# Kernel tuning notes

Hardware: AMD Instinct MI355X
Metric: run time of the kernel (lower is better)

Reference implementation:

```python
import jax, jax.numpy as jnp
import numpy as np
from jax import lax

NL, H, E, N, R, K, C, V, P = 8, 768, 1536, 16, 4, 4, 3, 256, 2048
EPS = 1e-5

def layernorm(x, w, b):
    m = jnp.mean(x, -1, keepdims=True)
    v = jnp.var(x, -1, keepdims=True)
    return (x - m) * lax.rsqrt(v + EPS) * w + b

def causal_dwconv(x, w, b):
    # x: [B,L,E], w: [E,K], b: [E]; causal depthwise conv (pad K-1 left, truncate)
    Bn, L, _ = x.shape
    xp = jnp.pad(x, ((0, 0), (K - 1, 0), (0, 0)))
    y = b
    acc = jnp.zeros_like(x)
    for j in range(K):
        acc = acc + xp[:, j:j + L, :] * w[:, j]
    return acc + b

def selective_scan(u, dt, Bm, Cm, A, Dv):
    # u,dt: [B,L,E]; Bm,Cm: [B,L,N]; A: [E,N]; Dv: [E]
    Bn = u.shape[0]
    def step(h, inp):
        u_t, dt_t, b_t, c_t = inp  # [B,E],[B,E],[B,N],[B,N]
        dA = jnp.exp(dt_t[:, :, None] * A)                      # [B,E,N]
        h = h * dA + (dt_t * u_t)[:, :, None] * b_t[:, None, :]
        y = jnp.einsum('ben,bn->be', h, c_t)
        return h, y
    h0 = jnp.zeros((Bn, E, N), dtype=u.dtype)
    xs = (u.transpose(1, 0, 2), dt.transpose(1, 0, 2),
          Bm.transpose(1, 0, 2), Cm.transpose(1, 0, 2))
    _, ys = lax.scan(step, h0, xs)
    return ys.transpose(1, 0, 2) + u * Dv

def mamba_block(hs, p):
    res = hs
    x = layernorm(hs, p['ln_w'], p['ln_b'])
    proj = x @ p['in_w'] + p['in_b']                            # [B,L,2E]
    xm, gate = proj[..., :E], proj[..., E:]
    xm = causal_dwconv(xm, p['conv_w'], p['conv_b'])
    u = jax.nn.silu(xm)                                         # swish activation in mixer
    dbc = u @ p['xproj_w']                                      # [B,L,R+2N]
    dt = jax.nn.softplus(dbc[..., :R] @ p['dt_w'] + p['dt_b'])  # [B,L,E]
    Bm, Cm = dbc[..., R:R + N], dbc[..., R + N:]
    A = -jnp.exp(p['A_log'])                                    # [E,N]
    y = selective_scan(u, dt, Bm, Cm, A, p['D'])
    y = jax.nn.sigmoid(gate) * y
    hs = y @ p['out_w'] + p['out_b'] + res
    # fractal layer: mean of recursive swish-linear branches, residual
    acc = jnp.zeros_like(hs)
    for i in range(C):
        yb = hs
        for _ in range(3):
            yb = jax.nn.silu(yb @ p['frac_w'][i] + p['frac_b'][i])
        acc = acc + yb
    return hs + 0.5 * acc / C

def setup_inputs() -> dict:
    key = jax.random.key(0)
    ks = jax.random.split(key, 20)
    s = lambda i, shp, sc=0.02: jax.random.normal(ks[i], shp, jnp.float32) * sc
    inp = {
        'input_ids': jax.random.randint(ks[0], (2, 2048), 0, V),
        'tok_emb': s(1, (V, H)),
        'pos_emb': s(2, (P, H)),
        'ln_w': jnp.ones((NL, H)), 'ln_b': jnp.zeros((NL, H)),
        'in_w': s(3, (NL, H, 2 * E)), 'in_b': jnp.zeros((NL, 2 * E)),
        'conv_w': s(4, (NL, E, K), 0.3), 'conv_b': jnp.zeros((NL, E)),
        'xproj_w': s(5, (NL, E, R + 2 * N)),
        'dt_w': s(6, (NL, R, E), 0.1),
        'dt_b': jnp.full((NL, E), -4.0),
        'A_log': jnp.tile(jnp.log(jnp.arange(1, N + 1, dtype=jnp.float32)), (NL, E, 1)),
        'D': jnp.ones((NL, E)),
        'out_w': s(7, (NL, E, H)), 'out_b': jnp.zeros((NL, H)),
        'frac_w': s(8, (NL, C, H, H)), 'frac_b': jnp.zeros((NL, C, H)),
        'fln_w': jnp.ones((H,)), 'fln_b': jnp.zeros((H,)),
    }
    return inp

def reference(input_ids, tok_emb, pos_emb, ln_w, ln_b, in_w, in_b, conv_w, conv_b,
              xproj_w, dt_w, dt_b, A_log, D, out_w, out_b, frac_w, frac_b, fln_w, fln_b):
    Bn, L = input_ids.shape
    hs = tok_emb[input_ids] + pos_emb[jnp.arange(L)][None]
    for l in range(NL):
        p = {'ln_w': ln_w[l], 'ln_b': ln_b[l], 'in_w': in_w[l], 'in_b': in_b[l],
             'conv_w': conv_w[l], 'conv_b': conv_b[l], 'xproj_w': xproj_w[l],
             'dt_w': dt_w[l], 'dt_b': dt_b[l], 'A_log': A_log[l], 'D': D[l],
             'out_w': out_w[l], 'out_b': out_b[l], 'frac_w': frac_w[l], 'frac_b': frac_b[l]}
        hs = mamba_block(hs, p)
    return layernorm(hs, fln_w, fln_b)
```

## Files before the change

### kernel.cpp

```cpp
#include <hip/hip_runtime.h>
#include <hip/hip_bf16.h>
#include <stdint.h>

#define NLAYER 8
#define HDIM   768
#define EDIM   1536
#define NST    16
#define LSEQ   2048
#define BATCH  2
#define BLTOK  (BATCH*LSEQ)
#define NCH    (BATCH*EDIM)
#define NCHK   64

typedef unsigned short u16;
typedef short  short8  __attribute__((ext_vector_type(8)));
typedef float  f32x4   __attribute__((ext_vector_type(4)));
typedef unsigned short u16x4 __attribute__((ext_vector_type(4)));

__device__ __forceinline__ float sigm(float x){ return 1.0f/(1.0f+__expf(-x)); }

__device__ __forceinline__ u16 bf16_rne(float x){
  unsigned u = __float_as_uint(x);
  return (u16)((u + 0x7fffu + ((u>>16)&1u)) >> 16);
}
__device__ __forceinline__ float bf16_f(u16 h){
  return __uint_as_float(((unsigned)h)<<16);
}

__device__ __forceinline__ void gload16(const void* g, void* l){
  __builtin_amdgcn_global_load_lds(
    reinterpret_cast<const __attribute__((address_space(1))) unsigned*>(
        reinterpret_cast<uintptr_t>(g)),
    reinterpret_cast<__attribute__((address_space(3))) unsigned*>(
        reinterpret_cast<uintptr_t>(l)),
    16, 0, 0);
}

__global__ __launch_bounds__(256) void wprep_k(
    const float* __restrict__ W, u16* __restrict__ H, u16* __restrict__ L,
    int Nsrc, int Ndst, int K)
{
  __shared__ float T[32][33];
  int z = blockIdx.z;
  W += (size_t)z*K*Nsrc; H += (size_t)z*Ndst*K; L += (size_t)z*Ndst*K;
  int n0 = blockIdx.x*32, k0 = blockIdx.y*32;
  int tx = threadIdx.x&31, ty = threadIdx.x>>5;
  #pragma unroll
  for (int r=0;r<4;r++){
    int kk = ty+8*r, col = n0+tx;
    T[kk][tx] = (col<Nsrc) ? W[(size_t)(k0+kk)*Nsrc+col] : 0.f;
  }
  __syncthreads();
  #pragma unroll
  for (int r=0;r<4;r++){
    int nn = ty+8*r, n = n0+nn, k = k0+tx;
    if (n<Ndst){
      float f = T[tx][nn];
      u16 h = bf16_rne(f);
      H[(size_t)n*K+k] = h;
      L[(size_t)n*K+k] = bf16_rne(f - bf16_f(h));
    }
  }
}

template<int EPI, int SPLIT, int SPLITK>
__global__ __launch_bounds__(256) void gemm_u(
    const u16* __restrict__ AH, const u16* __restrict__ AL, int lda,
    const u16* __restrict__ WH, const u16* __restrict__ WL, int ldw,
    const float* __restrict__ bias, void* __restrict__ Cout,
    int N, int Kloop, size_t zA, size_t zW, size_t zB, size_t zC)
{
  constexpr int NPL = (SPLIT==3)?4:2;
  constexpr int NLD = (SPLIT==3)?8:4;
  __shared__ __align__(16) u16 smem[2*NPL*4096];

  const int z = blockIdx.z;
  const u16* ah = AH + (size_t)z*zA;
  const u16* bh = WH + (size_t)z*zW;
  const u16* al = nullptr;
  const u16* bl = nullptr;
  if constexpr (SPLIT==3){ al = AL + (size_t)z*zA; bl = WL + (size_t)z*zW; }

  const int tid  = threadIdx.x;
  const int m0 = blockIdx.y<<7, n0 = blockIdx.x<<7;
  const int wave = tid>>6, lane = tid&63;
  const int r = lane&15, q = lane>>4;
  const int wm = (wave&1)<<6, wn = (wave>>1)<<6;
  const int srow = tid>>2;
  const int scol = (tid&3)*8;
  const int sdst = tid*8;

  const int nk = Kloop >> 5;

  auto STAGE = [&](int idx){
    u16* s = smem + (size_t)(idx&1)*NPL*4096;
    const int k0 = idx<<5;
    #pragma unroll
    for (int i=0;i<2;i++){
      const size_t gao = (size_t)(m0 + i*64 + srow)*lda + k0 + scol;
      const size_t gbo = (size_t)(n0 + i*64 + srow)*ldw + k0 + scol;
      const int lo = i*2048 + sdst;
      gload16(ah+gao, s+lo);
      gload16(bh+gbo, s+4096+lo);
      if constexpr (SPLIT==3){
        gload16(al+gao, s+2*4096+lo);
        gload16(bl+gbo, s+3*4096+lo);
      }
    }
  };

  f32x4 acc[4][4];
  #pragma unroll
  for (int i=0;i<4;i++)
    #pragma unroll
    for (int j=0;j<4;j++)
      #pragma unroll
      for (int t=0;t<4;t++) acc[i][j][t]=0.f;

  STAGE(0);
  if (nk > 1) STAGE(1);

  for (int idx = 0; idx < nk; idx++){
    if (idx+1 < nk) asm volatile("s_waitcnt vmcnt(%0)" :: "n"(NLD) : "memory");
    else            asm volatile("s_waitcnt vmcnt(0)" ::: "memory");
    __builtin_amdgcn_s_barrier();

    const u16* s = smem + (size_t)(idx&1)*NPL*4096;
    const u16* sA = s;
    const u16* sB = s + 4096;

    short8 aHf[4], bHf[4];
    #pragma unroll
    for (int i=0;i<4;i++) aHf[i] = *(const short8*)&sA[(wm + 16*i + r)*32 + q*8];
    #pragma unroll
    for (int j=0;j<4;j++) bHf[j] = *(const short8*)&sB[(wn + 16*j + r)*32 + q*8];
    short8 aLf[4], bLf[4];
    if constexpr (SPLIT==3){
      const u16* sAL = s + 2*4096;
      const u16* sBL = s + 3*4096;
      #pragma unroll
      for (int i=0;i<4;i++) aLf[i] = *(const short8*)&sAL[(wm + 16*i + r)*32 + q*8];
      #pragma unroll
      for (int j=0;j<4;j++) bLf[j] = *(const short8*)&sBL[(wn + 16*j + r)*32 + q*8];
    }
    asm volatile("s_waitcnt lgkmcnt(0)" ::: "memory");
    __builtin_amdgcn_sched_barrier(0);
    __builtin_amdgcn_s_barrier();

    if (idx+2 < nk) STAGE(idx+2);

    if constexpr (SPLIT==3){
      #pragma unroll
      for (int i=0;i<4;i++)
        #pragma unroll
        for (int j=0;j<4;j++){
          acc[i][j] = __builtin_amdgcn_mfma_f32_16x16x32_bf16(aHf[i], bHf[j], acc[i][j], 0,0,0);
          acc[i][j] = __builtin_amdgcn_mfma_f32_16x16x32_bf16(aHf[i], bLf[j], acc[i][j], 0,0,0);
          acc[i][j] = __builtin_amdgcn_mfma_f32_16x16x32_bf16(aLf[i], bHf[j], acc[i][j], 0,0,0);
        }
    } else {
      #pragma unroll
      for (int i=0;i<4;i++)
        #pragma unroll
        for (int j=0;j<4;j++)
          acc[i][j] = __builtin_amdgcn_mfma_f32_16x16x32_bf16(aHf[i], bHf[j], acc[i][j], 0,0,0);
    }
  }

  float* Cf = (float*)Cout + (size_t)z*zC;
  u16*   Cu = (u16*)Cout   + (size_t)z*zC;
  const float* bz = bias ? (bias + (size_t)z*zB) : bias;
  #pragma unroll
  for (int j=0;j<4;j++){
    int n_out = n0 + wn + 16*j + r;
    float bv = (bz && (!SPLITK || z==0)) ? bz[n_out] : 0.f;
    #pragma unroll
    for (int i=0;i<4;i++){
      #pragma unroll
      for (int reg=0;reg<4;reg++){
        int m_out = m0 + wm + 16*i + 4*q + reg;
        float v = acc[i][j][reg] + bv;
        if (EPI & 1) v *= sigm(v);
        size_t o = (size_t)m_out*N + n_out;
        if      (EPI & 16) atomicAdd(&Cf[o], v);
        else if (EPI & 8)  Cu[o] = bf16_rne(v);
        else if (EPI & 2)  Cf[o] += v;
        else               Cf[o] = v;
      }
    }
  }
}

__global__ __launch_bounds__(64) void xgemm_k(
    const float* __restrict__ A, const u16* __restrict__ XH,
    const u16* __restrict__ XL, float* __restrict__ DBC)
{
  int m0 = blockIdx.x*16;
  int lane = threadIdx.x;
  int r = lane&15, q = lane>>4;
  f32x4 acc[3];
  #pragma unroll
  for (int j=0;j<3;j++)
    #pragma unroll
    for (int t=0;t<4;t++) acc[j][t]=0.f;

  for (int k0 = 0; k0 < EDIM; k0 += 32){
    const float* ap = A + (size_t)(m0+r)*EDIM + k0 + q*8;
    float f[8];
    *(float4*)&f[0] = *(const float4*)(ap+0);
    *(float4*)&f[4] = *(const float4*)(ap+4);
    short8 ah, al;
    #pragma unroll
    for (int t=0;t<8;t++){
      u16 h = bf16_rne(f[t]);
      ah[t] = (short)h;
      al[t] = (short)bf16_rne(f[t]-bf16_f(h));
    }
    #pragma unroll
    for (int j=0;j<3;j++){
      size_t o = (size_t)(16*j+r)*EDIM + k0 + q*8;
      short8 bh = *(const short8*)&XH[o];
      short8 bl = *(const short8*)&XL[o];
      acc[j] = __builtin_amdgcn_mfma_f32_16x16x32_bf16(ah, bh, acc[j], 0,0,0);
      acc[j] = __builtin_amdgcn_mfma_f32_16x16x32_bf16(ah, bl, acc[j], 0,0,0);
      acc[j] = __builtin_amdgcn_mfma_f32_16x16x32_bf16(al, bh, acc[j], 0,0,0);
    }
  }
  #pragma unroll
  for (int j=0;j<3;j++){
    int n = 16*j + r;
    if (n < 36){
      #pragma unroll
      for (int reg=0;reg<4;reg++){
        int m = m0 + 4*q + reg;
        DBC[(size_t)m*36 + n] = acc[j][reg];
      }
    }
  }
}

__global__ __launch_bounds__(256) void embed_k(
    const int* __restrict__ ids, const float* __restrict__ tok,
    const float* __restrict__ pos, float* __restrict__ HS)
{
  int idx = blockIdx.x*256 + threadIdx.x;
  int h = idx % HDIM; int t = idx / HDIM;
  int lpos = t % LSEQ;
  int id = ids[t];
  HS[idx] = tok[id*HDIM + h] + pos[lpos*HDIM + h];
}

template<int PACK>
__global__ __launch_bounds__(256) void ln_k(
    const float* __restrict__ X, const float* __restrict__ w,
    const float* __restrict__ b, void* __restrict__ O1, void* __restrict__ O2)
{
  int t = blockIdx.x;
  const float* x = X + (size_t)t*HDIM;
  float s=0.f, s2=0.f;
  for (int i=threadIdx.x; i<HDIM; i+=256){ float v=x[i]; s+=v; s2+=v*v; }
  #pragma unroll
  for (int off=32; off; off>>=1){ s += __shfl_down(s,off,64); s2 += __shfl_down(s2,off,64); }
  __shared__ float rs[4], rs2[4], mv[2];
  int lane = threadIdx.x & 63, wv = threadIdx.x >> 6;
  if (!lane){ rs[wv]=s; rs2[wv]=s2; }
  __syncthreads();
  if (!threadIdx.x){
    float a = rs[0]+rs[1]+rs[2]+rs[3];
    float c = rs2[0]+rs2[1]+rs2[2]+rs2[3];
    float m = a/HDIM;
    mv[0]=m; mv[1]=rsqrtf(c/HDIM - m*m + 1e-5f);
  }
  __syncthreads();
  float m = mv[0], r = mv[1];
  for (int i=threadIdx.x; i<HDIM; i+=256){
    float v = (x[i]-m)*r*w[i] + b[i];
    if (PACK){
      u16 h = bf16_rne(v);
      ((u16*)O1)[(size_t)t*HDIM+i] = h;
      ((u16*)O2)[(size_t)t*HDIM+i] = bf16_rne(v - bf16_f(h));
    } else {
      ((float*)O1)[(size_t)t*HDIM+i] = v;
    }
  }
}

__global__ __launch_bounds__(256) void cvt_k(
    const float* __restrict__ X, u16* __restrict__ O)
{
  int i = blockIdx.x*256 + threadIdx.x;
  float4 v = ((const float4*)X)[i];
  u16x4 o;
  o[0]=bf16_rne(v.x); o[1]=bf16_rne(v.y); o[2]=bf16_rne(v.z); o[3]=bf16_rne(v.w);
  ((u16x4*)O)[i] = o;
}

__global__ __launch_bounds__(256) void conv_silu_k(
    const float* __restrict__ PROJ, const float* __restrict__ cw,
    const float* __restrict__ cb, float* __restrict__ U)
{
  int idx = blockIdx.x*256 + threadIdx.x;
  int e = idx % EDIM; int t = idx / EDIM;
  int l = t % LSEQ; int tb = t - l;
  float acc = cb[e];
  #pragma unroll
  for (int j=0;j<4;j++){
    int tt = l + j - 3;
    if (tt >= 0) acc += PROJ[(size_t)(tb+tt)*(2*EDIM) + e] * cw[e*4+j];
  }
  U[idx] = acc * sigm(acc);
}

__global__ __launch_bounds__(256) void scanA_k(
    const float* __restrict__ U, const float* __restrict__ DBC,
    const float* __restrict__ Alog, const float* __restrict__ dtw,
    const float* __restrict__ dtb, float* __restrict__ PSP,
    float* __restrict__ PSS)
{
  const int CH = LSEQ/NCHK;
  int el = threadIdx.x & 63, jj = threadIdx.x >> 6;
  int ch = blockIdx.x*64 + el;
  int j  = blockIdx.y*4 + jj;
  int e = ch % EDIM, b = ch / EDIM;

  float a[16], P[16], S[16];
  #pragma unroll
  for (int n=0;n<16;n++){ a[n] = -__expf(Alog[e*NST+n]); P[n]=1.f; S[n]=0.f; }
  float w0=dtw[e], w1=dtw[EDIM+e], w2=dtw[2*EDIM+e], w3=dtw[3*EDIM+e];
  float db=dtb[e];
  size_t base=(size_t)b*LSEQ;

  for (int t=j*CH; t<j*CH+CH; t++){
    size_t tok = base+t;
    float4 d4 = *(const float4*)&DBC[tok*36];
    float4 B0 = *(const float4*)&DBC[tok*36+4];
    float4 B1 = *(const float4*)&DBC[tok*36+8];
    float4 B2 = *(const float4*)&DBC[tok*36+12];
    float4 B3 = *(const float4*)&DBC[tok*36+16];
    float dt = d4.x*w0 + d4.y*w1 + d4.z*w2 + d4.w*w3 + db;
    dt = (dt>20.f)?dt:log1pf(__expf(dt));
    float du = dt * U[tok*EDIM+e];
    float Bv[16];
    *(float4*)&Bv[0]=B0; *(float4*)&Bv[4]=B1; *(float4*)&Bv[8]=B2; *(float4*)&Bv[12]=B3;
    #pragma unroll
    for (int n=0;n<16;n++){
      float dA = __expf(dt*a[n]);
      P[n]*=dA; S[n]=S[n]*dA + du*Bv[n];
    }
  }
  #pragma unroll
  for (int n=0;n<16;n++){
    PSP[(size_t)(j*16+n)*NCH + ch] = P[n];
    PSS[(size_t)(j*16+n)*NCH + ch] = S[n];
  }
}

__global__ __launch_bounds__(256) void scanB_k(
    const float* __restrict__ PSP, float* __restrict__ PSS)
{
  int idx = blockIdx.x*256 + threadIdx.x;
  int n = idx / NCH, ch = idx % NCH;
  float hin = 0.f;
  #pragma unroll 4
  for (int jj=0;jj<NCHK;jj++){
    size_t o = (size_t)(jj*16+n)*NCH + ch;
    float p = PSP[o], s = PSS[o];
    PSS[o] = hin;
    hin = p*hin + s;
  }
}

__global__ __launch_bounds__(256) void scanC_k(
    const float* __restrict__ U, const float* __restrict__ DBC,
    const float* __restrict__ Alog, const float* __restrict__ dtw,
    const float* __restrict__ dtb, const float* __restrict__ HIN,
    const float* __restrict__ Dp, const float* __restrict__ PROJ,
    u16* __restrict__ YH, u16* __restrict__ YL)
{
  const int CH = LSEQ/NCHK;
  int el = threadIdx.x & 63, jj = threadIdx.x >> 6;
  int ch = blockIdx.x*64 + el;
  int j  = blockIdx.y*4 + jj;
  int e = ch % EDIM, b = ch / EDIM;

  float a[16], h[16];
  #pragma unroll
  for (int n=0;n<16;n++){
    a[n] = -__expf(Alog[e*NST+n]);
    h[n] = HIN[(size_t)(j*16+n)*NCH + ch];
  }
  float w0=dtw[e], w1=dtw[EDIM+e], w2=dtw[2*EDIM+e], w3=dtw[3*EDIM+e];
  float db=dtb[e], dcf=Dp[e];
  size_t base=(size_t)b*LSEQ;

  for (int t=j*CH; t<j*CH+CH; t++){
    size_t tok = base+t;
    float4 d4 = *(const float4*)&DBC[tok*36];
    float4 B0 = *(const float4*)&DBC[tok*36+4];
    float4 B1 = *(const float4*)&DBC[tok*36+8];
    float4 B2 = *(const float4*)&DBC[tok*36+12];
    float4 B3 = *(const float4*)&DBC[tok*36+16];
    float4 C0 = *(const float4*)&DBC[tok*36+20];
    float4 C1 = *(const float4*)&DBC[tok*36+24];
    float4 C2 = *(const float4*)&DBC[tok*36+28];
    float4 C3 = *(const float4*)&DBC[tok*36+32];
    float dt = d4.x*w0 + d4.y*w1 + d4.z*w2 + d4.w*w3 + db;
    dt = (dt>20.f)?dt:log1pf(__expf(dt));
    float u = U[tok*EDIM+e];
    float du = dt * u;
    float Bv[16], Cv[16];
    *(float4*)&Bv[0]=B0; *(float4*)&Bv[4]=B1; *(float4*)&Bv[8]=B2; *(float4*)&Bv[12]=B3;
    *(float4*)&Cv[0]=C0; *(float4*)&Cv[4]=C1; *(float4*)&Cv[8]=C2; *(float4*)&Cv[12]=C3;
    float y = 0.f;
    #pragma unroll
    for (int n=0;n<16;n++){
      float dA = __expf(dt*a[n]);
      h[n] = h[n]*dA + du*Bv[n];
      y += h[n]*Cv[n];
    }
    float g = PROJ[tok*(2*EDIM) + EDIM + e];
    float yv = (y + u*dcf)*sigm(g);
    u16 hh = bf16_rne(yv);
    YH[tok*EDIM + e] = hh;
    YL[tok*EDIM + e] = bf16_rne(yv - bf16_f(hh));
  }
}

__global__ __launch_bounds__(256) void addscale3_k(
    float* __restrict__ HS, const float* __restrict__ FB)
{
  const size_t S = (size_t)BLTOK*HDIM;
  size_t i = blockIdx.x*256 + threadIdx.x;
  HS[i] += (FB[i] + FB[i+S] + FB[i+2*S]) * (0.5f/3.0f);
}

extern "C" void kernel_launch(void* const* d_in, const int* in_sizes, int n_in,
                              void* d_out, int out_size, void* d_ws, size_t ws_size,
                              hipStream_t stream)
{
  const int*   ids      = (const int*)d_in[0];
  const float* tok_emb  = (const float*)d_in[1];
  const float* pos_emb  = (const float*)d_in[2];
  const float* ln_w     = (const float*)d_in[3];
  const float* ln_b     = (const float*)d_in[4];
  const float* in_w     = (const float*)d_in[5];
  const float* in_b     = (const float*)d_in[6];
  const float* conv_w   = (const float*)d_in[7];
  const float* conv_b   = (const float*)d_in[8];
  const float* xproj_w  = (const float*)d_in[9];
  const float* dt_w     = (const float*)d_in[10];
  const float* dt_b     = (const float*)d_in[11];
  const float* A_log    = (const float*)d_in[12];
  const float* Dp       = (const float*)d_in[13];
  const float* out_w    = (const float*)d_in[14];
  const float* out_b    = (const float*)d_in[15];
  const float* frac_w   = (const float*)d_in[16];
  const float* frac_b   = (const float*)d_in[17];
  const float* fln_w    = (const float*)d_in[18];
  const float* fln_b    = (const float*)d_in[19];

  const size_t F_HS   = (size_t)BLTOK*HDIM;
  const size_t F_PROJ = (size_t)BLTOK*2*EDIM;
  const size_t F_R1   = (size_t)BLTOK*EDIM;
  float* HS   = (float*)d_ws;
  float* PROJ = HS   + F_HS;
  float* R1   = PROJ + F_PROJ;
  float* DBC  = R1   + F_R1;
  u16* W16  = (u16*)(DBC + (size_t)BLTOK*36);
  u16* inH  = W16;
  u16* inL  = inH  + (size_t)2359296;
  u16* outH = inL  + (size_t)2359296;
  u16* outL = outH + (size_t)1179648;
  u16* frH  = outL + (size_t)1179648;
  u16* frL  = frH  + (size_t)1769472;
  u16* xH   = frL  + (size_t)1769472;
  u16* xL   = xH   + (size_t)73728;
  float* PSP = (float*)(xL + (size_t)73728);
  float* PSS = PSP + (size_t)NCHK*16*NCH;
  u16* YH  = (u16*)(PSS + (size_t)NCHK*16*NCH);
  u16* YL  = YH + (size_t)BLTOK*EDIM;
  u16*   XH  = (u16*)R1;
  u16*   XL  = XH + F_HS;
  float* U   = R1;
  u16*   HSB = (u16*)PSP;
  float* FB  = PROJ;
  u16*   S1  = (u16*)(PROJ + 3*F_HS);
  u16*   S2  = S1 + 3*F_HS;

  embed_k<<<(BLTOK*HDIM)/256, 256, 0, stream>>>(ids, tok_emb, pos_emb, HS);

  const size_t zWf = (size_t)HDIM*HDIM;
  for (int l = 0; l < NLAYER; l++){
    wprep_k<<<dim3(3072/32, 768/32), 256, 0, stream>>>(
        in_w + (size_t)l*HDIM*2*EDIM, inH, inL, 2*EDIM, 2*EDIM, HDIM);
    wprep_k<<<dim3(768/32, 1536/32), 256, 0, stream>>>(
        out_w + (size_t)l*EDIM*HDIM, outH, outL, HDIM, HDIM, EDIM);
    wprep_k<<<dim3(768/32, 768/32, 3), 256, 0, stream>>>(
        frac_w + (size_t)l*3*HDIM*HDIM, frH, frL, HDIM, HDIM, HDIM);
    wprep_k<<<dim3(2, 1536/32), 256, 0, stream>>>(
        xproj_w + (size_t)l*EDIM*36, xH, xL, 36, 48, EDIM);

    ln_k<1><<<BLTOK, 256, 0, stream>>>(HS, ln_w + l*HDIM, ln_b + l*HDIM, XH, XL);

    gemm_u<0,3,0><<<dim3(24, 32), 256, 0, stream>>>(
        XH, XL, HDIM, inH, inL, HDIM, in_b + l*2*EDIM, PROJ,
        2*EDIM, HDIM, 0,0,0,0);

    conv_silu_k<<<(BLTOK*EDIM)/256, 256, 0, stream>>>(
        PROJ, conv_w + l*EDIM*4, conv_b + l*EDIM, U);

    xgemm_k<<<BLTOK/16, 64, 0, stream>>>(U, xH, xL, DBC);

    scanA_k<<<dim3(NCH/64, NCHK/4), 256, 0, stream>>>(
        U, DBC, A_log + (size_t)l*EDIM*NST, dt_w + (size_t)l*4*EDIM,
        dt_b + (size_t)l*EDIM, PSP, PSS);
    scanB_k<<<(NCH*16)/256, 256, 0, stream>>>(PSP, PSS);
    scanC_k<<<dim3(NCH/64, NCHK/4), 256, 0, stream>>>(
        U, DBC, A_log + (size_t)l*EDIM*NST, dt_w + (size_t)l*4*EDIM,
        dt_b + (size_t)l*EDIM, PSS, Dp + (size_t)l*EDIM, PROJ, YH, YL);

    gemm_u<16,3,1><<<dim3(6, 32, 2), 256, 0, stream>>>(
        YH, YL, EDIM, outH, outL, EDIM, out_b + l*HDIM, HS,
        HDIM, EDIM/2, EDIM/2, EDIM/2, 0, 0);

    cvt_k<<<(BLTOK*HDIM)/1024, 256, 0, stream>>>(HS, HSB);

    gemm_u<9,1,0><<<dim3(6, 32, 3), 256, 0, stream>>>(
        HSB, nullptr, HDIM, frH, frL, HDIM, frac_b + (size_t)l*3*HDIM, S1,
        HDIM, HDIM, 0, zWf, HDIM, F_HS);
    gemm_u<9,1,0><<<dim3(6, 32, 3), 256, 0, stream>>>(
        S1, nullptr, HDIM, frH, frL, HDIM, frac_b + (size_t)l*3*HDIM, S2,
        HDIM, HDIM, F_HS, zWf, HDIM, F_HS);
    gemm_u<1,1,0><<<dim3(6, 32, 3), 256, 0, stream>>>(
        S2, nullptr, HDIM, frH, frL, HDIM, frac_b + (size_t)l*3*HDIM, FB,
        HDIM, HDIM, F_HS, zWf, HDIM, F_HS);

    addscale3_k<<<(BLTOK*HDIM)/256, 256, 0, stream>>>(HS, FB);
  }

  ln_k<0><<<BLTOK, 256, 0, stream>>>(HS, fln_w, fln_b, (float*)d_out, nullptr);
}
```

Measured before the change: 3.855 ms.

## Double-buffer GEMM MFMA fragments in registers to overlap LDS reads with MFMA

```diff
diff --git a/kernel.cpp b/kernel.cpp
--- a/kernel.cpp
+++ b/kernel.cpp
@@ -109,6 +109,23 @@
     }
   };
 
+  short8 aH0[4], bH0[4], aL0[4], bL0[4];
+  short8 aH1[4], bH1[4], aL1[4], bL1[4];
+
+  auto LOADF = [&](short8* fa, short8* fb, short8* fc, short8* fd, int par){
+    const u16* s = smem + (size_t)par*NPL*4096;
+    #pragma unroll
+    for (int i=0;i<4;i++) fa[i] = *(const short8*)&s[(wm + 16*i + r)*32 + q*8];
+    #pragma unroll
+    for (int j=0;j<4;j++) fb[j] = *(const short8*)&s[4096 + (wn + 16*j + r)*32 + q*8];
+    if constexpr (SPLIT==3){
+      #pragma unroll
+      for (int i=0;i<4;i++) fc[i] = *(const short8*)&s[2*4096 + (wm + 16*i + r)*32 + q*8];
+      #pragma unroll
+      for (int j=0;j<4;j++) fd[j] = *(const short8*)&s[3*4096 + (wn + 16*j + r)*32 + q*8];
+    }
+  };
+
   f32x4 acc[4][4];
   #pragma unroll
   for (int i=0;i<4;i++)
@@ -117,55 +134,52 @@
       #pragma unroll
       for (int t=0;t<4;t++) acc[i][j][t]=0.f;
 
-  STAGE(0);
-  if (nk > 1) STAGE(1);
-
-  for (int idx = 0; idx < nk; idx++){
-    if (idx+1 < nk) asm volatile("s_waitcnt vmcnt(%0)" :: "n"(NLD) : "memory");
-    else            asm volatile("s_waitcnt vmcnt(0)" ::: "memory");
-    __builtin_amdgcn_s_barrier();
-
-    const u16* s = smem + (size_t)(idx&1)*NPL*4096;
-    const u16* sA = s;
-    const u16* sB = s + 4096;
-
-    short8 aHf[4], bHf[4];
-    #pragma unroll
-    for (int i=0;i<4;i++) aHf[i] = *(const short8*)&sA[(wm + 16*i + r)*32 + q*8];
-    #pragma unroll
-    for (int j=0;j<4;j++) bHf[j] = *(const short8*)&sB[(wn + 16*j + r)*32 + q*8];
-    short8 aLf[4], bLf[4];
-    if constexpr (SPLIT==3){
-      const u16* sAL = s + 2*4096;
-      const u16* sBL = s + 3*4096;
-      #pragma unroll
-      for (int i=0;i<4;i++) aLf[i] = *(const short8*)&sAL[(wm + 16*i + r)*32 + q*8];
-      #pragma unroll
-      for (int j=0;j<4;j++) bLf[j] = *(const short8*)&sBL[(wn + 16*j + r)*32 + q*8];
-    }
-    asm volatile("s_waitcnt lgkmcnt(0)" ::: "memory");
-    __builtin_amdgcn_sched_barrier(0);
-    __builtin_amdgcn_s_barrier();
-
-    if (idx+2 < nk) STAGE(idx+2);
-
+  auto MM = [&](short8* fa, short8* fb, short8* fc, short8* fd){
     if constexpr (SPLIT==3){
       #pragma unroll
       for (int i=0;i<4;i++)
         #pragma unroll
         for (int j=0;j<4;j++){
-          acc[i][j] = __builtin_amdgcn_mfma_f32_16x16x32_bf16(aHf[i], bHf[j], acc[i][j], 0,0,0);
-          acc[i][j] = __builtin_amdgcn_mfma_f32_16x16x32_bf16(aHf[i], bLf[j], acc[i][j], 0,0,0);
-          acc[i][j] = __builtin_amdgcn_mfma_f32_16x16x32_bf16(aLf[i], bHf[j], acc[i][j], 0,0,0);
+          acc[i][j] = __builtin_amdgcn_mfma_f32_16x16x32_bf16(fa[i], fb[j], acc[i][j], 0,0,0);
+          acc[i][j] = __builtin_amdgcn_mfma_f32_16x16x32_bf16(fa[i], fd[j], acc[i][j], 0,0,0);
+          acc[i][j] = __builtin_amdgcn_mfma_f32_16x16x32_bf16(fc[i], fb[j], acc[i][j], 0,0,0);
         }
     } else {
       #pragma unroll
       for (int i=0;i<4;i++)
         #pragma unroll
         for (int j=0;j<4;j++)
-          acc[i][j] = __builtin_amdgcn_mfma_f32_16x16x32_bf16(aHf[i], bHf[j], acc[i][j], 0,0,0);
-    }
-  }
+          acc[i][j] = __builtin_amdgcn_mfma_f32_16x16x32_bf16(fa[i], fb[j], acc[i][j], 0,0,0);
+    }
+  };
+
+  STAGE(0);
+  if (nk > 1){
+    STAGE(1);
+    asm volatile("s_waitcnt vmcnt(%0)" :: "n"(NLD) : "memory");
+  } else {
+    asm volatile("s_waitcnt vmcnt(0)" ::: "memory");
+  }
+  __builtin_amdgcn_s_barrier();
+  LOADF(aH0,bH0,aL0,bL0, 0);
+
+  #define GBODY(T, A,B,C,D, A2,B2,C2,D2)                              \
+    if ((T)+1 < nk){                                                  \
+      asm volatile("s_waitcnt lgkmcnt(0)" ::: "memory");              \
+      asm volatile("s_waitcnt vmcnt(0)" ::: "memory");                \
+      __builtin_amdgcn_s_barrier();                                   \
+      if ((T)+2 < nk) STAGE((T)+2);                                   \
+      LOADF(A2,B2,C2,D2, ((T)+1)&1);                                  \
+    }                                                                 \
+    MM(A,B,C,D);
+
+  int t = 0;
+  for (; t+1 < nk; t += 2){
+    GBODY(t,   aH0,bH0,aL0,bL0, aH1,bH1,aL1,bL1);
+    GBODY(t+1, aH1,bH1,aL1,bL1, aH0,bH0,aL0,bL0);
+  }
+  if (t < nk){ MM(aH0,bH0,aL0,bL0); }
+  #undef GBODY
 
   float* Cf = (float*)Cout + (size_t)z*zC;
   u16*   Cu = (u16*)Cout   + (size_t)z*zC;
```

After: 4.176 ms. 1.08x slower.
